# Performance work log

Hardware: AMD Instinct MI355X
Metric: run time of the kernel (lower is better)

## Reference

```python
import jax, jax.numpy as jnp
import numpy as np
import math

B, S, D, H = 2, 2048, 1024, 16
DK = D // H


def setup_inputs() -> dict:
    key = jax.random.key(0)
    ks = jax.random.split(key, 8)
    scale = 0.02
    f = lambda k, shape: jax.random.normal(k, shape, dtype=jnp.float32)
    causal = jnp.tril(jnp.ones((S, S), dtype=jnp.int32))  # [S,S]
    mask = jnp.broadcast_to(causal[None, None], (B, 1, S, S))
    return {
        "query": f(ks[0], (B, S, D)),
        "key_in": f(ks[1], (B, S, D)),
        "value": f(ks[2], (B, S, D)),
        "Wq": f(ks[3], (D, D)) * scale, "bq": jnp.zeros((D,), jnp.float32),
        "Wk": f(ks[4], (D, D)) * scale, "bk": jnp.zeros((D,), jnp.float32),
        "Wv": f(ks[5], (D, D)) * scale, "bv": jnp.zeros((D,), jnp.float32),
        "Wo": f(ks[6], (D, D)) * scale, "bo": jnp.zeros((D,), jnp.float32),
        "mask": mask,
    }


def reference(query, key_in, value, Wq, bq, Wk, bk, Wv, bv, Wo, bo, mask):
    # linear projections (torch Linear: x @ W.T + b), split into heads -> [B,H,S,DK]
    def proj(x, W, b):
        return (x @ W.T + b).reshape(B, -1, H, DK).transpose(0, 2, 1, 3)

    q = proj(query, Wq, bq)
    k = proj(key_in, Wk, bk)
    v = proj(value, Wv, bv)

    scores = jnp.einsum("bhqd,bhkd->bhqk", q, k) / math.sqrt(DK)  # [B,H,S,S]
    scores = jnp.where(mask.astype(bool), scores, -jnp.inf)
    attn = jax.nn.softmax(scores, axis=-1)
    x = jnp.einsum("bhqk,bhkd->bhqd", attn, v)  # [B,H,S,DK]
    x = x.transpose(0, 2, 1, 3).reshape(B, S, D)
    return x @ Wo.T + bo
```

## Files before the change

kernel.cpp:

```cpp
#include <hip/hip_runtime.h>
#include <hip/hip_bf16.h>

constexpr int Bc = 2, Sc = 2048, Dc = 1024, Hc = 16, DKc = 64;
constexpr int Nrows = Bc * Sc;
constexpr float QSC = 0.125f * 1.4426950408889634f;

typedef short bf16x8 __attribute__((ext_vector_type(8)));
typedef short bf16x4 __attribute__((ext_vector_type(4)));
typedef float floatx4 __attribute__((ext_vector_type(4)));
typedef unsigned short u16x8 __attribute__((ext_vector_type(8)));

__device__ __forceinline__ short f2bf(float f) {
    union { float f; unsigned u; } v; v.f = f;
    unsigned r = v.u + 0x7FFFu + ((v.u >> 16) & 1u);
    return (short)(r >> 16);
}

__device__ __forceinline__ void gld16(const void* g, void* l) {
    __builtin_amdgcn_global_load_lds((const __attribute__((address_space(1))) unsigned int*)g,
                                     (__attribute__((address_space(3))) unsigned int*)l,
                                     16, 0, 0);
}

__global__ __launch_bounds__(256) void cvt_bf16(
        const float* __restrict__ s0, const float* __restrict__ s1, const float* __restrict__ s2,
        const float* __restrict__ s3, const float* __restrict__ s4, const float* __restrict__ s5,
        const float* __restrict__ s6,
        short* __restrict__ d0, short* __restrict__ d1, short* __restrict__ d2,
        short* __restrict__ d3, short* __restrict__ d4, short* __restrict__ d5,
        short* __restrict__ d6) {
    const float* src; short* dst; int n;
    switch (blockIdx.y) {
        case 0: src = s0; dst = d0; n = Nrows * Dc; break;
        case 1: src = s1; dst = d1; n = Nrows * Dc; break;
        case 2: src = s2; dst = d2; n = Nrows * Dc; break;
        case 3: src = s3; dst = d3; n = Dc * Dc; break;
        case 4: src = s4; dst = d4; n = Dc * Dc; break;
        case 5: src = s5; dst = d5; n = Dc * Dc; break;
        default: src = s6; dst = d6; n = Dc * Dc; break;
    }
    const int stride = gridDim.x * 256 * 8;
    for (int i = (blockIdx.x * 256 + threadIdx.x) * 8; i < n; i += stride) {
        const float4 a = *(const float4*)(src + i);
        const float4 b = *(const float4*)(src + i + 4);
        u16x8 o;
        o[0] = (unsigned short)f2bf(a.x); o[1] = (unsigned short)f2bf(a.y);
        o[2] = (unsigned short)f2bf(a.z); o[3] = (unsigned short)f2bf(a.w);
        o[4] = (unsigned short)f2bf(b.x); o[5] = (unsigned short)f2bf(b.y);
        o[6] = (unsigned short)f2bf(b.z); o[7] = (unsigned short)f2bf(b.w);
        *(u16x8*)(dst + i) = o;
    }
}

template <int BM>
__device__ __forceinline__ void gemm_body(const short* __restrict__ A,
                                          const short* __restrict__ W,
                                          const float* __restrict__ bias,
                                          void* __restrict__ Cout,
                                          int mode, short* As, short* Ws) {
    constexpr int K = Dc, BK = 64;
    constexpr int MB = BM / 16;
    constexpr int A_BLKS = MB * 2;
    constexpr int TOT = A_BLKS + 16;
    constexpr int PER_W = TOT / 4;
    constexpr int WMB = MB / 2;

    const int tid  = threadIdx.x;
    const int w    = tid >> 6;
    const int lane = tid & 63;
    const int quad = lane >> 4;
    const int l15  = lane & 15;
    const int rowBase = blockIdx.y * BM;
    const int colBase = blockIdx.x * 128;
    const int wm = w >> 1, wn = w & 1;

    floatx4 acc[WMB][4];
#pragma unroll
    for (int j = 0; j < WMB; ++j)
#pragma unroll
        for (int t = 0; t < 4; ++t) acc[j][t] = (floatx4){0.f, 0.f, 0.f, 0.f};

    for (int k0 = 0; k0 < K; k0 += BK) {
        __syncthreads();
#pragma unroll
        for (int i = 0; i < PER_W; ++i) {
            const int blk = w * PER_W + i;
            if (blk < A_BLKS) {
                const int mb = blk >> 1, kh = blk & 1;
                const short* g = A + (size_t)(rowBase + mb * 16 + l15) * K + k0 + kh * 32 + quad * 8;
                gld16(g, As + blk * 512);
            } else {
                const int b2 = blk - A_BLKS;
                const int nb = b2 >> 1, kh = b2 & 1;
                const short* g = W + (size_t)(colBase + nb * 16 + l15) * K + k0 + kh * 32 + quad * 8;
                gld16(g, Ws + b2 * 512);
            }
        }
        __syncthreads();

        bf16x8 af[WMB][2], wf[4][2];
#pragma unroll
        for (int j = 0; j < WMB; ++j)
#pragma unroll
            for (int kh = 0; kh < 2; ++kh)
                af[j][kh] = *(const bf16x8*)(As + ((wm * WMB + j) * 2 + kh) * 512 + lane * 8);
#pragma unroll
        for (int t = 0; t < 4; ++t)
#pragma unroll
            for (int kh = 0; kh < 2; ++kh)
                wf[t][kh] = *(const bf16x8*)(Ws + ((wn * 4 + t) * 2 + kh) * 512 + lane * 8);

#pragma unroll
        for (int kh = 0; kh < 2; ++kh)
#pragma unroll
            for (int j = 0; j < WMB; ++j)
#pragma unroll
                for (int t = 0; t < 4; ++t)
                    acc[j][t] = __builtin_amdgcn_mfma_f32_16x16x32_bf16(af[j][kh], wf[t][kh], acc[j][t], 0, 0, 0);
    }

#pragma unroll
    for (int j = 0; j < WMB; ++j) {
#pragma unroll
        for (int t = 0; t < 4; ++t) {
            const int col = colBase + wn * 64 + t * 16 + l15;
            const float bv = bias[col];
            const int row0 = rowBase + (wm * WMB + j) * 16 + quad * 4;
            if (mode == 0) {
                float* Co = (float*)Cout;
#pragma unroll
                for (int r = 0; r < 4; ++r)
                    Co[(size_t)(row0 + r) * Dc + col] = acc[j][t][r] + bv;
            } else {
                short* Co = (short*)Cout;
                const int b = row0 >> 11;
                const int ss0 = row0 & (Sc - 1);
                const int h = col >> 6, dk = col & 63;
                if (mode == 1 || mode == 3) {
                    const float sc = (mode == 3) ? QSC : 1.0f;
#pragma unroll
                    for (int r = 0; r < 4; ++r)
                        Co[(((size_t)(b * Hc + h)) * Sc + ss0 + r) * DKc + dk] = f2bf((acc[j][t][r] + bv) * sc);
                } else {
                    short4 pk;
                    pk.x = f2bf(acc[j][t][0] + bv); pk.y = f2bf(acc[j][t][1] + bv);
                    pk.z = f2bf(acc[j][t][2] + bv); pk.w = f2bf(acc[j][t][3] + bv);
                    *(short4*)(Co + (((size_t)(b * Hc + h)) * DKc + dk) * Sc + ss0) = pk;
                }
            }
        }
    }
}

__global__ __launch_bounds__(256) void gemm_qkv(
        const short* __restrict__ Aq, const short* __restrict__ Ak, const short* __restrict__ Av,
        const short* __restrict__ Wq, const short* __restrict__ Wk, const short* __restrict__ Wv,
        const float* __restrict__ bq, const float* __restrict__ bk, const float* __restrict__ bv,
        short* __restrict__ Oq, short* __restrict__ Ok, short* __restrict__ Ov) {
    __shared__ short As[128 * 64];
    __shared__ short Ws[128 * 64];
    const int z = blockIdx.z;
    const short* A = (z == 0) ? Aq : (z == 1) ? Ak : Av;
    const short* W = (z == 0) ? Wq : (z == 1) ? Wk : Wv;
    const float* bs = (z == 0) ? bq : (z == 1) ? bk : bv;
    short* O = (z == 0) ? Oq : (z == 1) ? Ok : Ov;
    gemm_body<128>(A, W, bs, O, (z == 0) ? 3 : (z == 1) ? 1 : 2, As, Ws);
}

__global__ __launch_bounds__(256) void gemm_out(const short* __restrict__ A,
                                                const short* __restrict__ W,
                                                const float* __restrict__ bias,
                                                float* __restrict__ C) {
    __shared__ short As[64 * 64];
    __shared__ short Ws[128 * 64];
    gemm_body<64>(A, W, bias, C, 0, As, Ws);
}

__global__ __launch_bounds__(256) void flash_attn_mfma(const short* __restrict__ Qg,
                                                       const short* __restrict__ Kg,
                                                       const short* __restrict__ Vtg,
                                                       short* __restrict__ X) {
    __shared__ short KV[2][16 * 512];
    __shared__ short Pl[4][16 * 72];

    const int bh = blockIdx.x;
    const int qt = 31 - blockIdx.y;

    const int tid  = threadIdx.x;
    const int w    = tid >> 6;
    const int lane = tid & 63;
    const int quad = lane >> 4;
    const int l15  = lane & 15;

    const short* Qb = Qg  + (size_t)bh * Sc * DKc;
    const short* Kb = Kg  + (size_t)bh * Sc * DKc;
    const short* Vb = Vtg + (size_t)bh * DKc * Sc;

    bf16x8 qf[2];
    {
        const short* qp = Qb + (size_t)(qt * 64 + w * 16 + l15) * DKc + quad * 8;
        qf[0] = *(const bf16x8*)(qp);
        qf[1] = *(const bf16x8*)(qp + 32);
    }

    auto stage = [&](int kt, int buf) {
#pragma unroll
        for (int i = 0; i < 4; ++i) {
            const int blk = w * 4 + i;
            if (blk < 8) {
                const int t = blk >> 1, kh = blk & 1;
                gld16(Kb + (size_t)(kt * 64 + t * 16 + l15) * DKc + kh * 32 + quad * 8,
                      &KV[buf][blk * 512]);
            } else {
                const int b2 = blk - 8, dt = b2 >> 1, kh = b2 & 1;
                gld16(Vb + (size_t)(dt * 16 + l15) * Sc + kt * 64 + kh * 32 + quad * 8,
                      &KV[buf][blk * 512]);
            }
        }
    };

    floatx4 oacc[4];
#pragma unroll
    for (int t = 0; t < 4; ++t) oacc[t] = (floatx4){0.f, 0.f, 0.f, 0.f};
    float m_run = -1e30f, l_run = 0.f;
    const int qloc = w * 16 + l15;
    short* Pw = &Pl[w][0];

    stage(0, 0);

    for (int kt = 0; kt <= qt; ++kt) {
        const int cur = kt & 1;
        __syncthreads();
        if (kt < qt) stage(kt + 1, cur ^ 1);

        const short* Ks = &KV[cur][0];
        const short* Vs = &KV[cur][8 * 512];

        floatx4 sacc[4];
#pragma unroll
        for (int t = 0; t < 4; ++t) sacc[t] = (floatx4){0.f, 0.f, 0.f, 0.f};
#pragma unroll
        for (int t = 0; t < 4; ++t)
#pragma unroll
            for (int kh = 0; kh < 2; ++kh) {
                const bf16x8 af = *(const bf16x8*)(Ks + (t * 2 + kh) * 512 + lane * 8);
                sacc[t] = __builtin_amdgcn_mfma_f32_16x16x32_bf16(af, qf[kh], sacc[t], 0, 0, 0);
            }

        if (kt == qt) {
#pragma unroll
            for (int t = 0; t < 4; ++t)
#pragma unroll
                for (int r = 0; r < 4; ++r)
                    if ((t * 16 + quad * 4 + r) > qloc) sacc[t][r] = -1e30f;
        }

        float mt = sacc[0][0];
#pragma unroll
        for (int t = 0; t < 4; ++t)
#pragma unroll
            for (int r = 0; r < 4; ++r) mt = fmaxf(mt, sacc[t][r]);
        mt = fmaxf(mt, __shfl_xor(mt, 16));
        mt = fmaxf(mt, __shfl_xor(mt, 32));

        const float mn = fmaxf(m_run, mt);
        const float alpha = exp2f(m_run - mn);
        m_run = mn;

        float rs = 0.f;
#pragma unroll
        for (int t = 0; t < 4; ++t) {
            const float p0 = exp2f(sacc[t][0] - mn);
            const float p1 = exp2f(sacc[t][1] - mn);
            const float p2 = exp2f(sacc[t][2] - mn);
            const float p3 = exp2f(sacc[t][3] - mn);
            rs += (p0 + p1) + (p2 + p3);
            bf16x4 pk;
            pk[0] = f2bf(p0); pk[1] = f2bf(p1); pk[2] = f2bf(p2); pk[3] = f2bf(p3);
            *(bf16x4*)(Pw + l15 * 72 + t * 16 + quad * 4) = pk;
        }
        rs += __shfl_xor(rs, 16);
        rs += __shfl_xor(rs, 32);
        l_run = l_run * alpha + rs;
#pragma unroll
        for (int dt = 0; dt < 4; ++dt) oacc[dt] *= alpha;

        __asm__ __volatile__("s_waitcnt lgkmcnt(0)" ::: "memory");

        bf16x8 pb[2];
#pragma unroll
        for (int kh = 0; kh < 2; ++kh)
            pb[kh] = *(const bf16x8*)(Pw + l15 * 72 + kh * 32 + quad * 8);
#pragma unroll
        for (int kh = 0; kh < 2; ++kh)
#pragma unroll
            for (int dt = 0; dt < 4; ++dt) {
                const bf16x8 vf = *(const bf16x8*)(Vs + (dt * 2 + kh) * 512 + lane * 8);
                oacc[dt] = __builtin_amdgcn_mfma_f32_16x16x32_bf16(vf, pb[kh], oacc[dt], 0, 0, 0);
            }
    }

    const float inv = 1.0f / l_run;
    const int b = bh >> 4, h = bh & 15;
    const int qrow = qt * 64 + w * 16 + l15;
    short* Xr = X + ((size_t)b * Sc + qrow) * Dc + h * DKc;
#pragma unroll
    for (int dt = 0; dt < 4; ++dt) {
        short4 pk;
        pk.x = f2bf(oacc[dt][0] * inv);
        pk.y = f2bf(oacc[dt][1] * inv);
        pk.z = f2bf(oacc[dt][2] * inv);
        pk.w = f2bf(oacc[dt][3] * inv);
        *(short4*)(Xr + dt * 16 + quad * 4) = pk;
    }
}

extern "C" void kernel_launch(void* const* d_in, const int* in_sizes, int n_in,
                              void* d_out, int out_size, void* d_ws, size_t ws_size,
                              hipStream_t stream) {
    const float* query  = (const float*)d_in[0];
    const float* key_in = (const float*)d_in[1];
    const float* value  = (const float*)d_in[2];
    const float* Wq = (const float*)d_in[3];
    const float* bq = (const float*)d_in[4];
    const float* Wk = (const float*)d_in[5];
    const float* bk = (const float*)d_in[6];
    const float* Wv = (const float*)d_in[7];
    const float* bv = (const float*)d_in[8];
    const float* Wo = (const float*)d_in[9];
    const float* bo = (const float*)d_in[10];

    constexpr size_t TEN = (size_t)Nrows * Dc;
    constexpr size_t WTEN = (size_t)Dc * Dc;
    short* qbf = (short*)d_ws;
    short* kbf = qbf + TEN;
    short* vbf = kbf + TEN;
    short* wqb = vbf + TEN;
    short* wkb = wqb + WTEN;
    short* wvb = wkb + WTEN;
    short* wob = wvb + WTEN;
    short* Qh  = wob + WTEN;
    short* Kh  = Qh + TEN;
    short* Vt  = Kh + TEN;
    short* Xb  = Vt + TEN;

    cvt_bf16<<<dim3(512, 7), 256, 0, stream>>>(query, key_in, value, Wq, Wk, Wv, Wo,
                                               qbf, kbf, vbf, wqb, wkb, wvb, wob);

    gemm_qkv<<<dim3(Dc / 128, Nrows / 128, 3), 256, 0, stream>>>(
        qbf, kbf, vbf, wqb, wkb, wvb, bq, bk, bv, Qh, Kh, Vt);

    flash_attn_mfma<<<dim3(Bc * Hc, Sc / 64), 256, 0, stream>>>(Qh, Kh, Vt, Xb);

    gemm_out<<<dim3(Dc / 128, Nrows / 64), 256, 0, stream>>>(Xb, wob, bo, (float*)d_out);
}
```

Baseline: 287.0 us.

## Double-buffer GEMM LDS tiles with halved BK to overlap loads and MFMA

The shared GEMM body now uses two LDS buffers with a K-tile of 32 instead of one buffer with a K-tile of 64. The global-to-LDS load for the next tile is issued right after the barrier, so it runs while MFMAs consume the current tile. This cuts the barriers per iteration from two to one. The trade-off is twice as many iterations, each with only a few MFMAs per wave, which leaves little compute to hide the load latency behind.

```diff
diff --git a/kernel.cpp b/kernel.cpp
--- a/kernel.cpp
+++ b/kernel.cpp
@@ -58,12 +58,15 @@
                                           const float* __restrict__ bias,
                                           void* __restrict__ Cout,
                                           int mode, short* As, short* Ws) {
-    constexpr int K = Dc, BK = 64;
+    constexpr int K = Dc, BK = 32;
     constexpr int MB = BM / 16;
-    constexpr int A_BLKS = MB * 2;
-    constexpr int TOT = A_BLKS + 16;
+    constexpr int NB = 8;
+    constexpr int TOT = MB + NB;
     constexpr int PER_W = TOT / 4;
     constexpr int WMB = MB / 2;
+    constexpr int ASZ = MB * 512;
+    constexpr int WSZ = NB * 512;
+    constexpr int NIT = K / BK;
 
     const int tid  = threadIdx.x;
     const int w    = tid >> 6;
@@ -74,49 +77,49 @@
     const int colBase = blockIdx.x * 128;
     const int wm = w >> 1, wn = w & 1;
 
-    floatx4 acc[WMB][4];
-#pragma unroll
-    for (int j = 0; j < WMB; ++j)
-#pragma unroll
-        for (int t = 0; t < 4; ++t) acc[j][t] = (floatx4){0.f, 0.f, 0.f, 0.f};
-
-    for (int k0 = 0; k0 < K; k0 += BK) {
-        __syncthreads();
+    auto stage = [&](int k0, int buf) {
 #pragma unroll
         for (int i = 0; i < PER_W; ++i) {
             const int blk = w * PER_W + i;
-            if (blk < A_BLKS) {
-                const int mb = blk >> 1, kh = blk & 1;
-                const short* g = A + (size_t)(rowBase + mb * 16 + l15) * K + k0 + kh * 32 + quad * 8;
-                gld16(g, As + blk * 512);
+            if (blk < MB) {
+                gld16(A + (size_t)(rowBase + blk * 16 + l15) * K + k0 + quad * 8,
+                      As + buf * ASZ + blk * 512);
             } else {
-                const int b2 = blk - A_BLKS;
-                const int nb = b2 >> 1, kh = b2 & 1;
-                const short* g = W + (size_t)(colBase + nb * 16 + l15) * K + k0 + kh * 32 + quad * 8;
-                gld16(g, Ws + b2 * 512);
-            }
-        }
+                const int nb = blk - MB;
+                gld16(W + (size_t)(colBase + nb * 16 + l15) * K + k0 + quad * 8,
+                      Ws + buf * WSZ + nb * 512);
+            }
+        }
+    };
+
+    floatx4 acc[WMB][4];
+#pragma unroll
+    for (int j = 0; j < WMB; ++j)
+#pragma unroll
+        for (int t = 0; t < 4; ++t) acc[j][t] = (floatx4){0.f, 0.f, 0.f, 0.f};
+
+    stage(0, 0);
+
+    for (int kt = 0; kt < NIT; ++kt) {
+        const int cur = kt & 1;
         __syncthreads();
-
-        bf16x8 af[WMB][2], wf[4][2];
+        if (kt + 1 < NIT) stage((kt + 1) * BK, cur ^ 1);
+
+        const short* Ab = As + cur * ASZ;
+        const short* Wb = Ws + cur * WSZ;
+        bf16x8 af[WMB], wf[4];
 #pragma unroll
         for (int j = 0; j < WMB; ++j)
-#pragma unroll
-            for (int kh = 0; kh < 2; ++kh)
-                af[j][kh] = *(const bf16x8*)(As + ((wm * WMB + j) * 2 + kh) * 512 + lane * 8);
+            af[j] = *(const bf16x8*)(Ab + (wm * WMB + j) * 512 + lane * 8);
 #pragma unroll
         for (int t = 0; t < 4; ++t)
-#pragma unroll
-            for (int kh = 0; kh < 2; ++kh)
-                wf[t][kh] = *(const bf16x8*)(Ws + ((wn * 4 + t) * 2 + kh) * 512 + lane * 8);
-
-#pragma unroll
-        for (int kh = 0; kh < 2; ++kh)
-#pragma unroll
-            for (int j = 0; j < WMB; ++j)
-#pragma unroll
-                for (int t = 0; t < 4; ++t)
-                    acc[j][t] = __builtin_amdgcn_mfma_f32_16x16x32_bf16(af[j][kh], wf[t][kh], acc[j][t], 0, 0, 0);
+            wf[t] = *(const bf16x8*)(Wb + (wn * 4 + t) * 512 + lane * 8);
+
+#pragma unroll
+        for (int j = 0; j < WMB; ++j)
+#pragma unroll
+            for (int t = 0; t < 4; ++t)
+                acc[j][t] = __builtin_amdgcn_mfma_f32_16x16x32_bf16(af[j], wf[t], acc[j][t], 0, 0, 0);
     }
 
 #pragma unroll
@@ -157,8 +160,8 @@
         const short* __restrict__ Wq, const short* __restrict__ Wk, const short* __restrict__ Wv,
         const float* __restrict__ bq, const float* __restrict__ bk, const float* __restrict__ bv,
         short* __restrict__ Oq, short* __restrict__ Ok, short* __restrict__ Ov) {
-    __shared__ short As[128 * 64];
-    __shared__ short Ws[128 * 64];
+    __shared__ short As[2 * 8 * 512];
+    __shared__ short Ws[2 * 8 * 512];
     const int z = blockIdx.z;
     const short* A = (z == 0) ? Aq : (z == 1) ? Ak : Av;
     const short* W = (z == 0) ? Wq : (z == 1) ? Wk : Wv;
@@ -171,8 +174,8 @@
                                                 const short* __restrict__ W,
                                                 const float* __restrict__ bias,
                                                 float* __restrict__ C) {
-    __shared__ short As[64 * 64];
-    __shared__ short Ws[128 * 64];
+    __shared__ short As[2 * 4 * 512];
+    __shared__ short Ws[2 * 8 * 512];
     gemm_body<64>(A, W, bias, C, 0, As, Ws);
 }
 
```

Result: faster. 275.3 us (-4.1%).
